# Performance work log

Hardware: AMD Instinct MI355X
Metric: run time of the kernel (lower is better)

The kernel has to match this reference:

```python
import jax, jax.numpy as jnp
import numpy as np

TEMPERATURE = 0.5
EPS = 1e-12  # matches torch F.normalize default eps


def _l2_normalize(x):
    norm = jnp.sqrt(jnp.sum(x * x, axis=-1, keepdims=True))
    return x / jnp.maximum(norm, EPS)


def setup_inputs() -> dict:
    key = jax.random.key(0)
    k1, k2 = jax.random.split(key)
    B, C, D = 64, 512, 256
    visual_features = jax.random.normal(k1, (B, C, D), dtype=jnp.float32)
    text_embeddings = jax.random.normal(k2, (B, C, D), dtype=jnp.float32)
    return {"visual_features": visual_features, "text_embeddings": text_embeddings}


def reference(visual_features, text_embeddings):
    v = _l2_normalize(visual_features)   # (B, C, D)
    t = _l2_normalize(text_embeddings)   # (B, C, D)
    # positive: diagonal similarity per class
    sim_pos = jnp.einsum('bcd,bcd->bc', v, t)
    positive = jnp.exp(sim_pos / TEMPERATURE)            # (B, C)
    # full BxCxC similarity matrix
    all_sim = jnp.exp(jnp.einsum('bcd,bkd->bck', v, t) / TEMPERATURE)
    negative = jnp.sum(all_sim, axis=-1) - positive      # (B, C)
    loss = -jnp.log(positive / (positive + negative))
    return jnp.mean(loss)
```

## Files before the change

### kernel.cpp

```cpp
#include <hip/hip_runtime.h>
#include <hip/hip_bf16.h>

#define BB 64
#define CC 512
#define DD 256

typedef __attribute__((ext_vector_type(8))) short bf16x8;
typedef __attribute__((ext_vector_type(4))) float f32x4;
typedef unsigned int u32;

#define SWZ(r) (((r) & 7) << 4)

__device__ inline short f2bf(float f) {
    union { __hip_bfloat16 h; short s; } cv;
    cv.h = __float2bfloat16(f);
    return cv.s;
}

__global__ __launch_bounds__(256) void norm_rows(const float* __restrict__ in,
                                                 unsigned short* __restrict__ out) {
    const int row  = blockIdx.x * 4 + (threadIdx.x >> 6);
    const int lane = threadIdx.x & 63;
    const float4 x = reinterpret_cast<const float4*>(in)[(size_t)row * 64 + lane];
    float ss = x.x * x.x + x.y * x.y + x.z * x.z + x.w * x.w;
#pragma unroll
    for (int off = 32; off; off >>= 1) ss += __shfl_xor(ss, off);
    const float r = 1.0f / fmaxf(sqrtf(ss), 1e-12f);
    ushort4 o;
    o.x = (unsigned short)f2bf(x.x * r);
    o.y = (unsigned short)f2bf(x.y * r);
    o.z = (unsigned short)f2bf(x.z * r);
    o.w = (unsigned short)f2bf(x.w * r);
    reinterpret_cast<ushort4*>(out)[(size_t)row * 64 + lane] = o;
}

__global__ __launch_bounds__(512, 2) void gemm_loss(const float* __restrict__ V,
                                                    const unsigned short* __restrict__ Tn,
                                                    float* __restrict__ partials) {
    __shared__ char ldsb[65536];
    __shared__ float vred[256];
    __shared__ float dred[256];
    __shared__ float red2[2];

    const int i0    = blockIdx.x;
    const int inner = i0 & 63;
    const int b     = (inner & 7) * 8 + (inner >> 3);
    const int rb    = i0 >> 6;

    const int tid  = threadIdx.x;
    const int lane = tid & 63;
    const int wave = tid >> 6;
    const int wr   = wave >> 1;
    const int wc   = wave & 1;
    const int g    = lane >> 4;
    const int ln   = lane & 15;

    const float* gV = V + (size_t)b * (CC * DD) + (size_t)rb * 128 * DD;
    const char*  gT = reinterpret_cast<const char*>(Tn + (size_t)b * (CC * DD));

    {
        const int rrow  = tid >> 3;
        const int ecolB = (tid & 7) * 64;
#pragma unroll
        for (int p = 0; p < 2; ++p) {
            const int row = p * 64 + rrow;
            const float4* src =
                reinterpret_cast<const float4*>(gV + (size_t)row * DD) + (tid & 7) * 8;
            float4 x[8];
#pragma unroll
            for (int q = 0; q < 8; ++q) x[q] = src[q];
            float ss = 0.f;
#pragma unroll
            for (int q = 0; q < 8; ++q)
                ss += x[q].x * x[q].x + x[q].y * x[q].y + x[q].z * x[q].z + x[q].w * x[q].w;
            ss += __shfl_xor(ss, 1);
            ss += __shfl_xor(ss, 2);
            ss += __shfl_xor(ss, 4);
            const float rinv = 1.0f / fmaxf(sqrtf(ss), 1e-12f);
            char* dstrow = ldsb + row * 512;
            const int sw = SWZ(row);
#pragma unroll
            for (int q2 = 0; q2 < 4; ++q2) {
                const float4 v0 = x[2 * q2], v1 = x[2 * q2 + 1];
                bf16x8 o;
                o[0] = f2bf(v0.x * rinv); o[1] = f2bf(v0.y * rinv);
                o[2] = f2bf(v0.z * rinv); o[3] = f2bf(v0.w * rinv);
                o[4] = f2bf(v1.x * rinv); o[5] = f2bf(v1.y * rinv);
                o[6] = f2bf(v1.z * rinv); o[7] = f2bf(v1.w * rinv);
                *reinterpret_cast<bf16x8*>(dstrow + ((ecolB + q2 * 16) ^ sw)) = o;
            }
        }
    }
    __syncthreads();

    bf16x8 a[2][8];
#pragma unroll
    for (int i = 0; i < 2; ++i) {
        const int row  = wr * 32 + i * 16 + ln;
        const char* rp = ldsb + row * 512;
        const int sw   = SWZ(row);
#pragma unroll
        for (int kk = 0; kk < 8; ++kk)
            a[i][kk] = *reinterpret_cast<const bf16x8*>(rp + ((kk * 64 + g * 16) ^ sw));
    }
    __syncthreads();

    auto stage = [&](int t) {
        const char* gtile = gT + (size_t)t * 16384;
        char* dst = ldsb + (t % 3) * 16384 + wave * 2048;
#pragma unroll
        for (int r2 = 0; r2 < 2; ++r2) {
            const int L   = r2 * 1024 + (lane << 4);
            const int lr  = L >> 9;
            const int row = wave * 4 + lr;
            const int inrow = L & 511;
            __builtin_amdgcn_global_load_lds(
                (const u32*)(gtile + (size_t)row * 512 + (inrow ^ SWZ(row))),
                (u32*)(dst + r2 * 1024), 16, 0, 0);
        }
    };
    stage(0);
    stage(1);

    float rs[2][4];
    float dg[2][4];
#pragma unroll
    for (int i = 0; i < 2; ++i)
#pragma unroll
        for (int r = 0; r < 4; ++r) { rs[i][r] = 0.f; dg[i][r] = 0.f; }

    for (int t = 0; t < 16; ++t) {
        if (t < 15) asm volatile("s_waitcnt vmcnt(2)" ::: "memory");
        else        asm volatile("s_waitcnt vmcnt(0)" ::: "memory");
        __builtin_amdgcn_s_barrier();
        __builtin_amdgcn_sched_barrier(0);
        if (t < 14) stage(t + 2);

        const char* rp = ldsb + (t % 3) * 16384 + (wc * 16 + ln) * 512;
        const int sw   = SWZ(ln);
        f32x4 acc[2] = {(f32x4){0.f, 0.f, 0.f, 0.f}, (f32x4){0.f, 0.f, 0.f, 0.f}};
        __builtin_amdgcn_s_setprio(1);
#pragma unroll
        for (int kk = 0; kk < 8; ++kk) {
            const bf16x8 bb = *reinterpret_cast<const bf16x8*>(rp + ((kk * 64 + g * 16) ^ sw));
            acc[0] = __builtin_amdgcn_mfma_f32_16x16x32_bf16(a[0][kk], bb, acc[0], 0, 0, 0);
            acc[1] = __builtin_amdgcn_mfma_f32_16x16x32_bf16(a[1][kk], bb, acc[1], 0, 0, 0);
        }
        __builtin_amdgcn_s_setprio(0);

        const int gcol = t * 32 + wc * 16 + ln;
#pragma unroll
        for (int i = 0; i < 2; ++i) {
            const int grow = rb * 128 + wr * 32 + i * 16 + g * 4;
#pragma unroll
            for (int r = 0; r < 4; ++r) {
                const float s2 = acc[i][r] * 2.0f;
                rs[i][r] += __expf(s2);
                if (gcol == grow + r) dg[i][r] += s2;
            }
        }
    }

#pragma unroll
    for (int i = 0; i < 2; ++i)
#pragma unroll
        for (int r = 0; r < 4; ++r) {
            float v = rs[i][r];
            float d = dg[i][r];
#pragma unroll
            for (int m = 1; m < 16; m <<= 1) {
                v += __shfl_xor(v, m);
                d += __shfl_xor(d, m);
            }
            if (ln == 0) {
                const int rl = wr * 32 + i * 16 + g * 4 + r;
                vred[rl * 2 + wc] = v;
                dred[rl * 2 + wc] = d;
            }
        }
    __syncthreads();

    if (tid < 128) {
        const float vv = vred[tid * 2] + vred[tid * 2 + 1];
        const float dd = dred[tid * 2] + dred[tid * 2 + 1];
        float lsum = logf(vv) - dd;
#pragma unroll
        for (int m = 1; m < 64; m <<= 1) lsum += __shfl_xor(lsum, m);
        if (lane == 0) red2[wave] = lsum;
    }
    __syncthreads();
    if (tid == 0) partials[i0] = red2[0] + red2[1];
}

__global__ __launch_bounds__(256) void final_reduce(const float* __restrict__ partials,
                                                    float* __restrict__ out) {
    const int t = threadIdx.x;
    float v = partials[t];
#pragma unroll
    for (int m = 1; m < 64; m <<= 1) v += __shfl_xor(v, m);
    __shared__ float red[4];
    if ((t & 63) == 0) red[t >> 6] = v;
    __syncthreads();
    if (t == 0) out[0] = (red[0] + red[1] + red[2] + red[3]) * (1.0f / 32768.0f);
}

extern "C" void kernel_launch(void* const* d_in, const int* in_sizes, int n_in,
                              void* d_out, int out_size, void* d_ws, size_t ws_size,
                              hipStream_t stream) {
    const float* vis = (const float*)d_in[0];
    const float* txt = (const float*)d_in[1];

    unsigned short* Tn = (unsigned short*)d_ws;
    float* partials    = (float*)((char*)d_ws + (size_t)BB * CC * DD * 2);
    float* out         = (float*)d_out;

    norm_rows<<<8192, 256, 0, stream>>>(txt, Tn);
    gemm_loss<<<256, 512, 0, stream>>>(vis, Tn, partials);
    final_reduce<<<1, 256, 0, stream>>>(partials, out);
}
```

Measured before the change: 39.70 us.

## Double the column tile, deepen the T-tile pipeline, and skip the diagonal check off-block

Each iteration now processes 64 text columns instead of 32, with four 32KB LDS buffers in dynamic shared memory and three tiles prefetched ahead. Each wave issues four MFMAs per k-step, and the diagonal-match test runs only in the iteration that contains the block's diagonal. The aim is to halve loop iterations and barriers, keep more loads in flight, and trim exp-epilogue overhead. In exchange each block uses over 128KB of LDS, which allows only one block per CU and raises register pressure.

New measurement: 35.50 us. 10.6% less time.

```diff
diff --git a/kernel.cpp b/kernel.cpp
--- a/kernel.cpp
+++ b/kernel.cpp
@@ -34,13 +34,13 @@
     reinterpret_cast<ushort4*>(out)[(size_t)row * 64 + lane] = o;
 }
 
-__global__ __launch_bounds__(512, 2) void gemm_loss(const float* __restrict__ V,
+__global__ __launch_bounds__(512, 1) void gemm_loss(const float* __restrict__ V,
                                                     const unsigned short* __restrict__ Tn,
                                                     float* __restrict__ partials) {
-    __shared__ char ldsb[65536];
-    __shared__ float vred[256];
-    __shared__ float dred[256];
-    __shared__ float red2[2];
+    extern __shared__ char lds[];
+    float* vred = reinterpret_cast<float*>(lds + 131072);
+    float* dred = vred + 256;
+    float* red2 = dred + 256;
 
     const int i0    = blockIdx.x;
     const int inner = i0 & 63;
@@ -77,7 +77,7 @@
             ss += __shfl_xor(ss, 2);
             ss += __shfl_xor(ss, 4);
             const float rinv = 1.0f / fmaxf(sqrtf(ss), 1e-12f);
-            char* dstrow = ldsb + row * 512;
+            char* dstrow = lds + row * 512;
             const int sw = SWZ(row);
 #pragma unroll
             for (int q2 = 0; q2 < 4; ++q2) {
@@ -97,7 +97,7 @@
 #pragma unroll
     for (int i = 0; i < 2; ++i) {
         const int row  = wr * 32 + i * 16 + ln;
-        const char* rp = ldsb + row * 512;
+        const char* rp = lds + row * 512;
         const int sw   = SWZ(row);
 #pragma unroll
         for (int kk = 0; kk < 8; ++kk)
@@ -106,13 +106,13 @@
     __syncthreads();
 
     auto stage = [&](int t) {
-        const char* gtile = gT + (size_t)t * 16384;
-        char* dst = ldsb + (t % 3) * 16384 + wave * 2048;
-#pragma unroll
-        for (int r2 = 0; r2 < 2; ++r2) {
+        const char* gtile = gT + (size_t)t * 32768;
+        char* dst = lds + (t & 3) * 32768 + wave * 4096;
+#pragma unroll
+        for (int r2 = 0; r2 < 4; ++r2) {
             const int L   = r2 * 1024 + (lane << 4);
             const int lr  = L >> 9;
-            const int row = wave * 4 + lr;
+            const int row = wave * 8 + lr;
             const int inrow = L & 511;
             __builtin_amdgcn_global_load_lds(
                 (const u32*)(gtile + (size_t)row * 512 + (inrow ^ SWZ(row))),
@@ -121,6 +121,7 @@
     };
     stage(0);
     stage(1);
+    stage(2);
 
     float rs[2][4];
     float dg[2][4];
@@ -129,35 +130,60 @@
 #pragma unroll
         for (int r = 0; r < 4; ++r) { rs[i][r] = 0.f; dg[i][r] = 0.f; }
 
-    for (int t = 0; t < 16; ++t) {
-        if (t < 15) asm volatile("s_waitcnt vmcnt(2)" ::: "memory");
-        else        asm volatile("s_waitcnt vmcnt(0)" ::: "memory");
+    for (int t = 0; t < 8; ++t) {
+        if (t < 6)      asm volatile("s_waitcnt vmcnt(8)" ::: "memory");
+        else if (t == 6) asm volatile("s_waitcnt vmcnt(4)" ::: "memory");
+        else            asm volatile("s_waitcnt vmcnt(0)" ::: "memory");
         __builtin_amdgcn_s_barrier();
         __builtin_amdgcn_sched_barrier(0);
-        if (t < 14) stage(t + 2);
-
-        const char* rp = ldsb + (t % 3) * 16384 + (wc * 16 + ln) * 512;
-        const int sw   = SWZ(ln);
-        f32x4 acc[2] = {(f32x4){0.f, 0.f, 0.f, 0.f}, (f32x4){0.f, 0.f, 0.f, 0.f}};
+        if (t < 5) stage(t + 3);
+
+        const char* bufp = lds + (t & 3) * 32768;
+        const int row0 = wc * 32 + ln;
+        const int row1 = wc * 32 + 16 + ln;
+        const char* rp0 = bufp + row0 * 512;
+        const char* rp1 = bufp + row1 * 512;
+        const int sw0 = SWZ(row0), sw1 = SWZ(row1);
+        f32x4 acc[2][2];
+#pragma unroll
+        for (int i = 0; i < 2; ++i)
+#pragma unroll
+            for (int j = 0; j < 2; ++j) acc[i][j] = (f32x4){0.f, 0.f, 0.f, 0.f};
         __builtin_amdgcn_s_setprio(1);
 #pragma unroll
         for (int kk = 0; kk < 8; ++kk) {
-            const bf16x8 bb = *reinterpret_cast<const bf16x8*>(rp + ((kk * 64 + g * 16) ^ sw));
-            acc[0] = __builtin_amdgcn_mfma_f32_16x16x32_bf16(a[0][kk], bb, acc[0], 0, 0, 0);
-            acc[1] = __builtin_amdgcn_mfma_f32_16x16x32_bf16(a[1][kk], bb, acc[1], 0, 0, 0);
+            const int ko = kk * 64 + g * 16;
+            const bf16x8 b0 = *reinterpret_cast<const bf16x8*>(rp0 + (ko ^ sw0));
+            const bf16x8 b1 = *reinterpret_cast<const bf16x8*>(rp1 + (ko ^ sw1));
+            acc[0][0] = __builtin_amdgcn_mfma_f32_16x16x32_bf16(a[0][kk], b0, acc[0][0], 0, 0, 0);
+            acc[1][0] = __builtin_amdgcn_mfma_f32_16x16x32_bf16(a[1][kk], b0, acc[1][0], 0, 0, 0);
+            acc[0][1] = __builtin_amdgcn_mfma_f32_16x16x32_bf16(a[0][kk], b1, acc[0][1], 0, 0, 0);
+            acc[1][1] = __builtin_amdgcn_mfma_f32_16x16x32_bf16(a[1][kk], b1, acc[1][1], 0, 0, 0);
         }
         __builtin_amdgcn_s_setprio(0);
 
-        const int gcol = t * 32 + wc * 16 + ln;
-#pragma unroll
-        for (int i = 0; i < 2; ++i) {
-            const int grow = rb * 128 + wr * 32 + i * 16 + g * 4;
-#pragma unroll
-            for (int r = 0; r < 4; ++r) {
-                const float s2 = acc[i][r] * 2.0f;
-                rs[i][r] += __expf(s2);
-                if (gcol == grow + r) dg[i][r] += s2;
-            }
+        if ((t >> 1) == rb) {
+#pragma unroll
+            for (int i = 0; i < 2; ++i) {
+                const int grow = rb * 128 + wr * 32 + i * 16 + g * 4;
+#pragma unroll
+                for (int j = 0; j < 2; ++j) {
+                    const int gcol = t * 64 + wc * 32 + j * 16 + ln;
+#pragma unroll
+                    for (int r = 0; r < 4; ++r) {
+                        const float s2 = acc[i][j][r] * 2.0f;
+                        rs[i][r] += __expf(s2);
+                        if (gcol == grow + r) dg[i][r] += s2;
+                    }
+                }
+            }
+        } else {
+#pragma unroll
+            for (int i = 0; i < 2; ++i)
+#pragma unroll
+                for (int j = 0; j < 2; ++j)
+#pragma unroll
+                    for (int r = 0; r < 4; ++r) rs[i][r] += __expf(acc[i][j][r] * 2.0f);
         }
     }
 
@@ -214,7 +240,11 @@
     float* partials    = (float*)((char*)d_ws + (size_t)BB * CC * DD * 2);
     float* out         = (float*)d_out;
 
+    const int lds_bytes = 131072 + 256 * 4 + 256 * 4 + 16;
+    hipFuncSetAttribute((const void*)gemm_loss, hipFuncAttributeMaxDynamicSharedMemorySize,
+                        lds_bytes);
+
     norm_rows<<<8192, 256, 0, stream>>>(txt, Tn);
-    gemm_loss<<<256, 512, 0, stream>>>(vis, Tn, partials);
+    gemm_loss<<<256, 512, lds_bytes, stream>>>(vis, Tn, partials);
     final_reduce<<<1, 256, 0, stream>>>(partials, out);
 }
```
